# Kernel optimization log

Measured on AMD Instinct MI355X. Metric: run time of the kernel, lower is better.

The kernel has to match this reference:

```python
import jax, jax.numpy as jnp
import numpy as np

VOCAB, EMBED, HIDDEN, NCLS = 50257, 64, 64, 5
B, S = 4096, 512
BN_EPS = 1e-5


def setup_inputs() -> dict:
    key = jax.random.key(0)
    ks = jax.random.split(key, 10)
    x = jax.random.randint(ks[0], (B, S), 0, VOCAB, dtype=jnp.int64 if jax.config.jax_enable_x64 else jnp.int32)
    emb = jax.random.normal(ks[1], (VOCAB, EMBED), dtype=jnp.float32)
    emb = emb.at[0].set(0.0)  # padding_idx=0
    s = 1.0 / np.sqrt(HIDDEN)
    W_ih = jax.random.uniform(ks[2], (HIDDEN, EMBED), minval=-s, maxval=s, dtype=jnp.float32)
    W_hh = jax.random.uniform(ks[3], (HIDDEN, HIDDEN), minval=-s, maxval=s, dtype=jnp.float32)
    b_ih = jax.random.uniform(ks[4], (HIDDEN,), minval=-s, maxval=s, dtype=jnp.float32)
    b_hh = jax.random.uniform(ks[5], (HIDDEN,), minval=-s, maxval=s, dtype=jnp.float32)
    gamma = jnp.ones((HIDDEN,), dtype=jnp.float32)
    beta = jnp.zeros((HIDDEN,), dtype=jnp.float32)
    sf = 1.0 / np.sqrt(HIDDEN)
    W_fc = jax.random.uniform(ks[6], (NCLS, HIDDEN), minval=-sf, maxval=sf, dtype=jnp.float32)
    b_fc = jax.random.uniform(ks[7], (NCLS,), minval=-sf, maxval=sf, dtype=jnp.float32)
    return {"x": x, "emb": emb, "W_ih": W_ih, "W_hh": W_hh, "b_ih": b_ih,
            "b_hh": b_hh, "gamma": gamma, "beta": beta, "W_fc": W_fc, "b_fc": b_fc}


def reference(x, emb, W_ih, W_hh, b_ih, b_hh, gamma, beta, W_fc, b_fc):
    # embedding gather: [B, S, E]
    xe = emb[x]
    # precompute input projection once: [B, S, H] -> scan over time as [S, B, H]
    xp = jnp.einsum('bse,he->bsh', xe, W_ih) + b_ih + b_hh
    xp_t = jnp.swapaxes(xp, 0, 1)

    def step(h, xt):
        h = jnp.tanh(xt + h @ W_hh.T)
        return h, None

    h0 = jnp.zeros((x.shape[0], HIDDEN), dtype=xp.dtype)
    h_n, _ = jax.lax.scan(step, h0, xp_t)

    # BatchNorm1d (training-mode math: batch stats, biased variance)
    mean = jnp.mean(h_n, axis=0)
    var = jnp.mean((h_n - mean) ** 2, axis=0)
    h_bn = (h_n - mean) * jax.lax.rsqrt(var + BN_EPS) * gamma + beta
    # dropout is identity in eval / deterministic reference
    logits = h_bn @ W_fc.T + b_fc  # [B, 5]
    return logits
```

## Files before the change

kernel.cpp:

```cpp
#include <hip/hip_runtime.h>

typedef _Float16 f16;
typedef __attribute__((ext_vector_type(4))) _Float16 f16x4;
typedef __attribute__((ext_vector_type(8))) _Float16 f16x8;
typedef __attribute__((ext_vector_type(4))) float f32x4;

constexpr int BATCH  = 4096;
constexpr int SEQ    = 512;
constexpr int HID    = 64;
constexpr int EMB_N4 = 50257 * 64 / 4;
constexpr float LOG2E2 = 2.8853900817779268f;

#define MFMA_K32(a, b, c) __builtin_amdgcn_mfma_f32_16x16x32_f16(a, b, c, 0, 0, 0)

__global__ __launch_bounds__(256) void prep_kernel(
    const float4* __restrict__ emb4, const float* __restrict__ Wih,
    const float* __restrict__ Whh, f16x4* __restrict__ emb_f4,
    f16* __restrict__ wih_f, f16* __restrict__ whh_f, float* __restrict__ bn_acc)
{
  int gid = blockIdx.x * 256 + threadIdx.x;
  if (gid < EMB_N4) {
    float4 v = emb4[gid];
    f16x4 o = {(f16)v.x, (f16)v.y, (f16)v.z, (f16)v.w};
    emb_f4[gid] = o;
  } else if (gid < EMB_N4 + 1024) {
    int i0 = (gid - EMB_N4) * 4;
    #pragma unroll
    for (int k = 0; k < 4; ++k) {
      int i = i0 + k;
      wih_f[i] = (f16)(Wih[i] * LOG2E2);
      whh_f[i] = (f16)(Whh[i] * LOG2E2);
    }
  } else if (gid < EMB_N4 + 1024 + 128) {
    bn_acc[gid - (EMB_N4 + 1024)] = 0.f;
  }
}

__global__ __launch_bounds__(64, 1) void rnn_scan_kernel(
    const int* __restrict__ xx, const f16* __restrict__ emb,
    const f16* __restrict__ wih, const f16* __restrict__ whh,
    const float* __restrict__ b_ih, const float* __restrict__ b_hh,
    float* __restrict__ hT , float* __restrict__ bn_acc)
{
  const int L = threadIdx.x;
  const int n = L & 15;
  const int q = L >> 4;
  const int R0 = blockIdx.x << 4;

  f16x8 Wi[4][2], Wp[4][2];
  f32x4 bias[4];
  #pragma unroll
  for (int f = 0; f < 4; ++f) {
    const f16* wr = whh + (16 * f + n) * 64;
    #pragma unroll
    for (int h = 0; h < 2; ++h) {
      f16x4 lo = *(const f16x4*)(wr + 32 * h + 4 * q);
      f16x4 hi = *(const f16x4*)(wr + 32 * h + 16 + 4 * q);
      Wp[f][h] = __builtin_shufflevector(lo, hi, 0, 1, 2, 3, 4, 5, 6, 7);
    }
    const f16* wi = wih + (16 * f + n) * 64;
    Wi[f][0] = *(const f16x8*)(wi + 8 * q);
    Wi[f][1] = *(const f16x8*)(wi + 32 + 8 * q);
    float4 bi = *(const float4*)(b_ih + 16 * f + 4 * q);
    float4 bh = *(const float4*)(b_hh + 16 * f + 4 * q);
    f32x4 b = {(bi.x + bh.x) * LOG2E2, (bi.y + bh.y) * LOG2E2,
               (bi.z + bh.z) * LOG2E2, (bi.w + bh.w) * LOG2E2};
    bias[f] = b;
  }

  f16x8 hB01 = {0, 0, 0, 0, 0, 0, 0, 0};
  f16x8 hB23 = {0, 0, 0, 0, 0, 0, 0, 0};

  const int4* x4 = (const int4*)(xx + (R0 + n) * SEQ);
  int4 K1 = x4[1];

  f16x8 e0[4], e1[4];
  {
    int4 K0 = x4[0];
    const int id0[4] = {K0.x, K0.y, K0.z, K0.w};
    #pragma unroll
    for (int u = 0; u < 4; ++u) {
      const f16* eb = emb + (long)id0[u] * 64 + 8 * q;
      e0[u] = *(const f16x8*)(eb);
      e1[u] = *(const f16x8*)(eb + 32);
    }
  }

  for (int t = 0; t < SEQ / 4; ++t) {
    int4 K2 = x4[(t + 2 < SEQ / 4) ? t + 2 : SEQ / 4 - 1];
    const int nid[4] = {K1.x, K1.y, K1.z, K1.w};
    const bool lastt = (t == SEQ / 4 - 1);

    #pragma unroll
    for (int u = 0; u < 4; ++u) {
      f32x4 D0 = MFMA_K32(Wi[0][0], e0[u], bias[0]);
      f32x4 D1 = MFMA_K32(Wi[1][0], e0[u], bias[1]);
      f32x4 D2 = MFMA_K32(Wi[2][0], e0[u], bias[2]);
      f32x4 D3 = MFMA_K32(Wi[3][0], e0[u], bias[3]);
      D0 = MFMA_K32(Wi[0][1], e1[u], D0);
      D1 = MFMA_K32(Wi[1][1], e1[u], D1);
      D2 = MFMA_K32(Wi[2][1], e1[u], D2);
      D3 = MFMA_K32(Wi[3][1], e1[u], D3);

      {
        const f16* eb = emb + (long)nid[u] * 64 + 8 * q;
        e0[u] = *(const f16x8*)(eb);
        e1[u] = *(const f16x8*)(eb + 32);
      }

      D0 = MFMA_K32(Wp[0][0], hB01, D0);
      D1 = MFMA_K32(Wp[1][0], hB01, D1);
      D2 = MFMA_K32(Wp[2][0], hB01, D2);
      D3 = MFMA_K32(Wp[3][0], hB01, D3);
      D0 = MFMA_K32(Wp[0][1], hB23, D0);
      D1 = MFMA_K32(Wp[1][1], hB23, D1);
      D2 = MFMA_K32(Wp[2][1], hB23, D2);
      D3 = MFMA_K32(Wp[3][1], hB23, D3);

      float th[4][4];
      #pragma unroll
      for (int r = 0; r < 4; ++r) {
        float e0f = __builtin_amdgcn_exp2f(D0[r]);
        float e1f = __builtin_amdgcn_exp2f(D1[r]);
        float e2f = __builtin_amdgcn_exp2f(D2[r]);
        float e3f = __builtin_amdgcn_exp2f(D3[r]);
        th[0][r] = fmaf(-2.0f, __builtin_amdgcn_rcpf(e0f + 1.0f), 1.0f);
        th[1][r] = fmaf(-2.0f, __builtin_amdgcn_rcpf(e1f + 1.0f), 1.0f);
        th[2][r] = fmaf(-2.0f, __builtin_amdgcn_rcpf(e2f + 1.0f), 1.0f);
        th[3][r] = fmaf(-2.0f, __builtin_amdgcn_rcpf(e3f + 1.0f), 1.0f);
        hB01[r]     = (f16)th[0][r];
        hB01[4 + r] = (f16)th[1][r];
        hB23[r]     = (f16)th[2][r];
        hB23[4 + r] = (f16)th[3][r];
      }

      if (lastt && u == 3) {
        #pragma unroll
        for (int f = 0; f < 4; ++f) {
          #pragma unroll
          for (int r = 0; r < 4; ++r) {
            float v = th[f][r];
            const int feat = 16 * f + 4 * q + r;
            hT[feat * BATCH + R0 + n] = v;
            float s1 = v, s2 = v * v;
            s1 += __shfl_xor(s1, 1, 64);  s2 += __shfl_xor(s2, 1, 64);
            s1 += __shfl_xor(s1, 2, 64);  s2 += __shfl_xor(s2, 2, 64);
            s1 += __shfl_xor(s1, 4, 64);  s2 += __shfl_xor(s2, 4, 64);
            s1 += __shfl_xor(s1, 8, 64);  s2 += __shfl_xor(s2, 8, 64);
            if (n == 0) {
              atomicAdd(bn_acc + feat, s1);
              atomicAdd(bn_acc + 64 + feat, s2);
            }
          }
        }
      }
    }
    K1 = K2;
  }
}

__global__ __launch_bounds__(256) void head_kernel(
    const float* __restrict__ hT, const float* __restrict__ bn_acc,
    const float* __restrict__ gamma, const float* __restrict__ beta,
    const float* __restrict__ Wfc, const float* __restrict__ bfc,
    float* __restrict__ out)
{
  __shared__ float sc[64], sh[64];
  const int tid = threadIdx.x;
  if (tid < 64) {
    float mean = bn_acc[tid] * (1.0f / BATCH);
    float var  = bn_acc[64 + tid] * (1.0f / BATCH) - mean * mean;
    float inv  = rsqrtf(var + 1e-5f);
    float s    = gamma[tid] * inv;
    sc[tid] = s;
    sh[tid] = beta[tid] - mean * s;
  }
  __syncthreads();
  const int b = blockIdx.x * 256 + tid;
  float acc[5];
  #pragma unroll
  for (int c = 0; c < 5; ++c) acc[c] = bfc[c];
  for (int j = 0; j < HID; ++j) {
    float hv  = hT[j * BATCH + b];
    float hat = fmaf(hv, sc[j], sh[j]);
    #pragma unroll
    for (int c = 0; c < 5; ++c) acc[c] = fmaf(hat, Wfc[c * 64 + j], acc[c]);
  }
  #pragma unroll
  for (int c = 0; c < 5; ++c) out[b * 5 + c] = acc[c];
}

extern "C" void kernel_launch(void* const* d_in, const int* in_sizes, int n_in,
                              void* d_out, int out_size, void* d_ws, size_t ws_size,
                              hipStream_t stream)
{
  const int*   x     = (const int*)d_in[0];
  const float* emb   = (const float*)d_in[1];
  const float* W_ih  = (const float*)d_in[2];
  const float* W_hh  = (const float*)d_in[3];
  const float* b_ih  = (const float*)d_in[4];
  const float* b_hh  = (const float*)d_in[5];
  const float* gamma = (const float*)d_in[6];
  const float* beta  = (const float*)d_in[7];
  const float* W_fc  = (const float*)d_in[8];
  const float* b_fc  = (const float*)d_in[9];

  char* ws = (char*)d_ws;
  float* hT     = (float*)ws;
  float* bn_acc = (float*)(ws + 1048576);
  f16*   emb_f  = (f16*)(ws + 1049088);
  f16*   wih_f  = (f16*)(ws + 7481984);
  f16*   whh_f  = (f16*)(ws + 7490176);

  const int prep_items = EMB_N4 + 1024 + 128;
  prep_kernel<<<dim3((prep_items + 255) / 256), dim3(256), 0, stream>>>(
      (const float4*)emb, W_ih, W_hh, (f16x4*)emb_f, wih_f, whh_f, bn_acc);
  rnn_scan_kernel<<<dim3(BATCH / 16), dim3(64), 0, stream>>>(
      x, emb_f, wih_f, whh_f, b_ih, b_hh, hT, bn_acc);
  head_kernel<<<dim3(BATCH / 256), dim3(256), 0, stream>>>(
      hT, bn_acc, gamma, beta, W_fc, b_fc, (float*)d_out);
}
```

Baseline: 284.7 us.

## Precompute projected embedding table and split recurrence across two waves

The prep kernel now projects the whole vocabulary through W_ih plus biases once (emb·W_ih^T), so the scan gathers pre-projected rows and skips the input-projection MFMAs each step. The scan block grows to two wavefronts, each owning half of the hidden features. They exchange their halves of h through double-buffered shared memory with a barrier every timestep. This removes half the per-wave MFMA chain and all input MFMAs, but adds a workgroup barrier plus LDS round trip on the serial critical path, and a larger prep GEMM over the vocabulary.

```diff
diff --git a/kernel.cpp b/kernel.cpp
--- a/kernel.cpp
+++ b/kernel.cpp
@@ -8,83 +8,83 @@
 constexpr int BATCH  = 4096;
 constexpr int SEQ    = 512;
 constexpr int HID    = 64;
-constexpr int EMB_N4 = 50257 * 64 / 4;
+constexpr int VOCAB  = 50257;
 constexpr float LOG2E2 = 2.8853900817779268f;
 
 #define MFMA_K32(a, b, c) __builtin_amdgcn_mfma_f32_16x16x32_f16(a, b, c, 0, 0, 0)
 
 __global__ __launch_bounds__(256) void prep_kernel(
-    const float4* __restrict__ emb4, const float* __restrict__ Wih,
-    const float* __restrict__ Whh, f16x4* __restrict__ emb_f4,
-    f16* __restrict__ wih_f, f16* __restrict__ whh_f, float* __restrict__ bn_acc)
-{
-  int gid = blockIdx.x * 256 + threadIdx.x;
-  if (gid < EMB_N4) {
-    float4 v = emb4[gid];
-    f16x4 o = {(f16)v.x, (f16)v.y, (f16)v.z, (f16)v.w};
-    emb_f4[gid] = o;
-  } else if (gid < EMB_N4 + 1024) {
-    int i0 = (gid - EMB_N4) * 4;
-    #pragma unroll
-    for (int k = 0; k < 4; ++k) {
-      int i = i0 + k;
-      wih_f[i] = (f16)(Wih[i] * LOG2E2);
-      whh_f[i] = (f16)(Whh[i] * LOG2E2);
-    }
-  } else if (gid < EMB_N4 + 1024 + 128) {
-    bn_acc[gid - (EMB_N4 + 1024)] = 0.f;
-  }
-}
-
-__global__ __launch_bounds__(64, 1) void rnn_scan_kernel(
-    const int* __restrict__ xx, const f16* __restrict__ emb,
-    const f16* __restrict__ wih, const f16* __restrict__ whh,
-    const float* __restrict__ b_ih, const float* __restrict__ b_hh,
+    const float* __restrict__ emb, const float* __restrict__ Wih,
+    const float* __restrict__ Whh, const float* __restrict__ bih,
+    const float* __restrict__ bhh,
+    f16* __restrict__ embP, f16* __restrict__ whh_f, float* __restrict__ bn_acc)
+{
+  const int gid = blockIdx.x * 256 + threadIdx.x;
+  if (gid < VOCAB * 64) {
+    const int v = gid >> 6, f = gid & 63;
+    const float4* er = (const float4*)(emb + v * 64);
+    const float4* wr = (const float4*)(Wih + f * 64);
+    float acc = bih[f] + bhh[f];
+    #pragma unroll
+    for (int k = 0; k < 16; ++k) {
+      float4 e = er[k], wv = wr[k];
+      acc = fmaf(e.x, wv.x, acc); acc = fmaf(e.y, wv.y, acc);
+      acc = fmaf(e.z, wv.z, acc); acc = fmaf(e.w, wv.w, acc);
+    }
+    embP[gid] = (f16)(acc * LOG2E2);
+  } else if (gid < VOCAB * 64 + 4096) {
+    const int i = gid - VOCAB * 64;
+    whh_f[i] = (f16)(Whh[i] * LOG2E2);
+  } else if (gid < VOCAB * 64 + 4096 + 128) {
+    bn_acc[gid - (VOCAB * 64 + 4096)] = 0.f;
+  }
+}
+
+__global__ __launch_bounds__(128, 1) void rnn_scan_kernel(
+    const int* __restrict__ xx, const f16* __restrict__ embP,
+    const f16* __restrict__ whh,
     float* __restrict__ hT , float* __restrict__ bn_acc)
 {
-  const int L = threadIdx.x;
+  __shared__ int4 xslot[2][2][64];
+  const int tid = threadIdx.x;
+  const int w = tid >> 6;
+  const int L = tid & 63;
   const int n = L & 15;
   const int q = L >> 4;
   const int R0 = blockIdx.x << 4;
 
-  f16x8 Wi[4][2], Wp[4][2];
-  f32x4 bias[4];
+  f16x8 Wp[2][2];
   #pragma unroll
-  for (int f = 0; f < 4; ++f) {
-    const f16* wr = whh + (16 * f + n) * 64;
-    #pragma unroll
-    for (int h = 0; h < 2; ++h) {
-      f16x4 lo = *(const f16x4*)(wr + 32 * h + 4 * q);
-      f16x4 hi = *(const f16x4*)(wr + 32 * h + 16 + 4 * q);
-      Wp[f][h] = __builtin_shufflevector(lo, hi, 0, 1, 2, 3, 4, 5, 6, 7);
-    }
-    const f16* wi = wih + (16 * f + n) * 64;
-    Wi[f][0] = *(const f16x8*)(wi + 8 * q);
-    Wi[f][1] = *(const f16x8*)(wi + 32 + 8 * q);
-    float4 bi = *(const float4*)(b_ih + 16 * f + 4 * q);
-    float4 bh = *(const float4*)(b_hh + 16 * f + 4 * q);
-    f32x4 b = {(bi.x + bh.x) * LOG2E2, (bi.y + bh.y) * LOG2E2,
-               (bi.z + bh.z) * LOG2E2, (bi.w + bh.w) * LOG2E2};
-    bias[f] = b;
-  }
-
-  f16x8 hB01 = {0, 0, 0, 0, 0, 0, 0, 0};
-  f16x8 hB23 = {0, 0, 0, 0, 0, 0, 0, 0};
+  for (int j = 0; j < 2; ++j) {
+    const f16* wr = whh + (16 * (2 * w + j) + n) * 64;
+    #pragma unroll
+    for (int c = 0; c < 2; ++c) {
+      f16x4 lo = *(const f16x4*)(wr + 32 * c + 4 * q);
+      f16x4 hi = *(const f16x4*)(wr + 32 * c + 16 + 4 * q);
+      Wp[j][c] = __builtin_shufflevector(lo, hi, 0, 1, 2, 3, 4, 5, 6, 7);
+    }
+  }
+
+  f16x8 hOwn = {0, 0, 0, 0, 0, 0, 0, 0};
+  xslot[0][w][L] = int4{0, 0, 0, 0};
 
   const int4* x4 = (const int4*)(xx + (R0 + n) * SEQ);
   int4 K1 = x4[1];
 
-  f16x8 e0[4], e1[4];
+  const f16* ebase = embP + 32 * w + 4 * q;
+  f16x4 ep0[4], ep1[4];
   {
     int4 K0 = x4[0];
     const int id0[4] = {K0.x, K0.y, K0.z, K0.w};
     #pragma unroll
     for (int u = 0; u < 4; ++u) {
-      const f16* eb = emb + (long)id0[u] * 64 + 8 * q;
-      e0[u] = *(const f16x8*)(eb);
-      e1[u] = *(const f16x8*)(eb + 32);
-    }
-  }
+      const f16* eb = ebase + (long)id0[u] * 64;
+      ep0[u] = *(const f16x4*)(eb);
+      ep1[u] = *(const f16x4*)(eb + 16);
+    }
+  }
+
+  asm volatile("s_waitcnt lgkmcnt(0)\n\ts_barrier" ::: "memory");
 
   for (int t = 0; t < SEQ / 4; ++t) {
     int4 K2 = x4[(t + 2 < SEQ / 4) ? t + 2 : SEQ / 4 - 1];
@@ -93,54 +93,47 @@
 
     #pragma unroll
     for (int u = 0; u < 4; ++u) {
-      f32x4 D0 = MFMA_K32(Wi[0][0], e0[u], bias[0]);
-      f32x4 D1 = MFMA_K32(Wi[1][0], e0[u], bias[1]);
-      f32x4 D2 = MFMA_K32(Wi[2][0], e0[u], bias[2]);
-      f32x4 D3 = MFMA_K32(Wi[3][0], e0[u], bias[3]);
-      D0 = MFMA_K32(Wi[0][1], e1[u], D0);
-      D1 = MFMA_K32(Wi[1][1], e1[u], D1);
-      D2 = MFMA_K32(Wi[2][1], e1[u], D2);
-      D3 = MFMA_K32(Wi[3][1], e1[u], D3);
-
-      {
-        const f16* eb = emb + (long)nid[u] * 64 + 8 * q;
-        e0[u] = *(const f16x8*)(eb);
-        e1[u] = *(const f16x8*)(eb + 32);
-      }
-
-      D0 = MFMA_K32(Wp[0][0], hB01, D0);
-      D1 = MFMA_K32(Wp[1][0], hB01, D1);
-      D2 = MFMA_K32(Wp[2][0], hB01, D2);
-      D3 = MFMA_K32(Wp[3][0], hB01, D3);
-      D0 = MFMA_K32(Wp[0][1], hB23, D0);
-      D1 = MFMA_K32(Wp[1][1], hB23, D1);
-      D2 = MFMA_K32(Wp[2][1], hB23, D2);
-      D3 = MFMA_K32(Wp[3][1], hB23, D3);
-
-      float th[4][4];
+      const int p = u & 1;
+      int4 oraw = xslot[p][w ^ 1][L];
+
+      f32x4 D0, D1;
       #pragma unroll
       for (int r = 0; r < 4; ++r) {
-        float e0f = __builtin_amdgcn_exp2f(D0[r]);
-        float e1f = __builtin_amdgcn_exp2f(D1[r]);
-        float e2f = __builtin_amdgcn_exp2f(D2[r]);
-        float e3f = __builtin_amdgcn_exp2f(D3[r]);
-        th[0][r] = fmaf(-2.0f, __builtin_amdgcn_rcpf(e0f + 1.0f), 1.0f);
-        th[1][r] = fmaf(-2.0f, __builtin_amdgcn_rcpf(e1f + 1.0f), 1.0f);
-        th[2][r] = fmaf(-2.0f, __builtin_amdgcn_rcpf(e2f + 1.0f), 1.0f);
-        th[3][r] = fmaf(-2.0f, __builtin_amdgcn_rcpf(e3f + 1.0f), 1.0f);
-        hB01[r]     = (f16)th[0][r];
-        hB01[4 + r] = (f16)th[1][r];
-        hB23[r]     = (f16)th[2][r];
-        hB23[4 + r] = (f16)th[3][r];
+        D0[r] = (float)ep0[u][r];
+        D1[r] = (float)ep1[u][r];
+      }
+
+      D0 = MFMA_K32(Wp[0][w], hOwn, D0);
+      D1 = MFMA_K32(Wp[1][w], hOwn, D1);
+
+      {
+        const f16* eb = ebase + (long)nid[u] * 64;
+        ep0[u] = *(const f16x4*)(eb);
+        ep1[u] = *(const f16x4*)(eb + 16);
+      }
+
+      union { int4 i; f16x8 h; } cv; cv.i = oraw;
+      D0 = MFMA_K32(Wp[0][w ^ 1], cv.h, D0);
+      D1 = MFMA_K32(Wp[1][w ^ 1], cv.h, D1);
+
+      float th[2][4];
+      #pragma unroll
+      for (int r = 0; r < 4; ++r) {
+        float ea = __builtin_amdgcn_exp2f(D0[r]);
+        float eb2 = __builtin_amdgcn_exp2f(D1[r]);
+        th[0][r] = fmaf(-2.0f, __builtin_amdgcn_rcpf(ea + 1.0f), 1.0f);
+        th[1][r] = fmaf(-2.0f, __builtin_amdgcn_rcpf(eb2 + 1.0f), 1.0f);
+        hOwn[r]     = (f16)th[0][r];
+        hOwn[4 + r] = (f16)th[1][r];
       }
 
       if (lastt && u == 3) {
         #pragma unroll
-        for (int f = 0; f < 4; ++f) {
+        for (int j = 0; j < 2; ++j) {
           #pragma unroll
           for (int r = 0; r < 4; ++r) {
-            float v = th[f][r];
-            const int feat = 16 * f + 4 * q + r;
+            float v = th[j][r];
+            const int feat = 16 * (2 * w + j) + 4 * q + r;
             hT[feat * BATCH + R0 + n] = v;
             float s1 = v, s2 = v * v;
             s1 += __shfl_xor(s1, 1, 64);  s2 += __shfl_xor(s2, 1, 64);
@@ -154,6 +147,11 @@
           }
         }
       }
+
+      union { f16x8 h; int4 i; } cw; cw.h = hOwn;
+      xslot[p ^ 1][w][L] = cw.i;
+
+      asm volatile("s_waitcnt lgkmcnt(0)\n\ts_barrier" ::: "memory");
     }
     K1 = K2;
   }
@@ -208,15 +206,14 @@
   char* ws = (char*)d_ws;
   float* hT     = (float*)ws;
   float* bn_acc = (float*)(ws + 1048576);
-  f16*   emb_f  = (f16*)(ws + 1049088);
-  f16*   wih_f  = (f16*)(ws + 7481984);
-  f16*   whh_f  = (f16*)(ws + 7490176);
-
-  const int prep_items = EMB_N4 + 1024 + 128;
+  f16*   embP   = (f16*)(ws + 1049088);
+  f16*   whh_f  = (f16*)(ws + 7481984);
+
+  const int prep_items = VOCAB * 64 + 4096 + 128;
   prep_kernel<<<dim3((prep_items + 255) / 256), dim3(256), 0, stream>>>(
-      (const float4*)emb, W_ih, W_hh, (f16x4*)emb_f, wih_f, whh_f, bn_acc);
-  rnn_scan_kernel<<<dim3(BATCH / 16), dim3(64), 0, stream>>>(
-      x, emb_f, wih_f, whh_f, b_ih, b_hh, hT, bn_acc);
+      emb, W_ih, W_hh, b_ih, b_hh, embP, whh_f, bn_acc);
+  rnn_scan_kernel<<<dim3(BATCH / 16), dim3(128), 0, stream>>>(
+      x, embP, whh_f, hT, bn_acc);
   head_kernel<<<dim3(BATCH / 256), dim3(256), 0, stream>>>(
       hT, bn_acc, gamma, beta, W_fc, b_fc, (float*)d_out);
 }
```

Result: slower. 356.1 us (+25.1%).

## Software-pipeline input projection ahead of recurrence and batch tanh reciprocals

Applied to the files above, without the earlier changes.

Computes the input-projection MFMAs for the next timestep after the current recurrent MFMAs, so each step's dependent chain holds only the eight W_hh MFMAs and the tanh. The tanh now shares one reciprocal across four values through a prefix-product trick, with exp2 inputs clamped to avoid overflow, which cuts transcendental instructions but lengthens the dependent multiply chain. The h fragment layout is changed to interleave the f-tiles, and the W_hh register shuffle is permuted to match.

```diff
diff --git a/kernel.cpp b/kernel.cpp
--- a/kernel.cpp
+++ b/kernel.cpp
@@ -21,8 +21,7 @@
   int gid = blockIdx.x * 256 + threadIdx.x;
   if (gid < EMB_N4) {
     float4 v = emb4[gid];
-    f16x4 o = {(f16)v.x, (f16)v.y, (f16)v.z, (f16)v.w};
-    emb_f4[gid] = o;
+    emb_f4[gid] = (f16x4){(f16)v.x, (f16)v.y, (f16)v.z, (f16)v.w};
   } else if (gid < EMB_N4 + 1024) {
     int i0 = (gid - EMB_N4) * 4;
     #pragma unroll
@@ -51,21 +50,20 @@
   f32x4 bias[4];
   #pragma unroll
   for (int f = 0; f < 4; ++f) {
-    const f16* wr = whh + (16 * f + n) * 64;
-    #pragma unroll
-    for (int h = 0; h < 2; ++h) {
-      f16x4 lo = *(const f16x4*)(wr + 32 * h + 4 * q);
-      f16x4 hi = *(const f16x4*)(wr + 32 * h + 16 + 4 * q);
-      Wp[f][h] = __builtin_shufflevector(lo, hi, 0, 1, 2, 3, 4, 5, 6, 7);
-    }
     const f16* wi = wih + (16 * f + n) * 64;
     Wi[f][0] = *(const f16x8*)(wi + 8 * q);
     Wi[f][1] = *(const f16x8*)(wi + 32 + 8 * q);
+    const f16* wr = whh + (16 * f + n) * 64;
+    #pragma unroll
+    for (int c = 0; c < 2; ++c) {
+      f16x4 lo = *(const f16x4*)(wr + 32 * c + 4 * q);
+      f16x4 hi = *(const f16x4*)(wr + 32 * c + 16 + 4 * q);
+      Wp[f][c] = __builtin_shufflevector(lo, hi, 0, 4, 1, 5, 2, 6, 3, 7);
+    }
     float4 bi = *(const float4*)(b_ih + 16 * f + 4 * q);
     float4 bh = *(const float4*)(b_hh + 16 * f + 4 * q);
-    f32x4 b = {(bi.x + bh.x) * LOG2E2, (bi.y + bh.y) * LOG2E2,
-               (bi.z + bh.z) * LOG2E2, (bi.w + bh.w) * LOG2E2};
-    bias[f] = b;
+    bias[f] = (f32x4){(bi.x + bh.x) * LOG2E2, (bi.y + bh.y) * LOG2E2,
+                      (bi.z + bh.z) * LOG2E2, (bi.w + bh.w) * LOG2E2};
   }
 
   f16x8 hB01 = {0, 0, 0, 0, 0, 0, 0, 0};
@@ -86,6 +84,13 @@
     }
   }
 
+  f32x4 Dip[4];
+  #pragma unroll
+  for (int f = 0; f < 4; ++f) {
+    Dip[f] = MFMA_K32(Wi[f][0], e0[0], bias[f]);
+    Dip[f] = MFMA_K32(Wi[f][1], e1[0], Dip[f]);
+  }
+
   for (int t = 0; t < SEQ / 4; ++t) {
     int4 K2 = x4[(t + 2 < SEQ / 4) ? t + 2 : SEQ / 4 - 1];
     const int nid[4] = {K1.x, K1.y, K1.z, K1.w};
@@ -93,14 +98,23 @@
 
     #pragma unroll
     for (int u = 0; u < 4; ++u) {
-      f32x4 D0 = MFMA_K32(Wi[0][0], e0[u], bias[0]);
-      f32x4 D1 = MFMA_K32(Wi[1][0], e0[u], bias[1]);
-      f32x4 D2 = MFMA_K32(Wi[2][0], e0[u], bias[2]);
-      f32x4 D3 = MFMA_K32(Wi[3][0], e0[u], bias[3]);
-      D0 = MFMA_K32(Wi[0][1], e1[u], D0);
-      D1 = MFMA_K32(Wi[1][1], e1[u], D1);
-      D2 = MFMA_K32(Wi[2][1], e1[u], D2);
-      D3 = MFMA_K32(Wi[3][1], e1[u], D3);
+      f32x4 D0 = MFMA_K32(Wp[0][0], hB01, Dip[0]);
+      f32x4 D1 = MFMA_K32(Wp[1][0], hB01, Dip[1]);
+      f32x4 D2 = MFMA_K32(Wp[2][0], hB01, Dip[2]);
+      f32x4 D3 = MFMA_K32(Wp[3][0], hB01, Dip[3]);
+      D0 = MFMA_K32(Wp[0][1], hB23, D0);
+      D1 = MFMA_K32(Wp[1][1], hB23, D1);
+      D2 = MFMA_K32(Wp[2][1], hB23, D2);
+      D3 = MFMA_K32(Wp[3][1], hB23, D3);
+
+      {
+        const int v = (u + 1) & 3;
+        #pragma unroll
+        for (int f = 0; f < 4; ++f) {
+          Dip[f] = MFMA_K32(Wi[f][0], e0[v], bias[f]);
+          Dip[f] = MFMA_K32(Wi[f][1], e1[v], Dip[f]);
+        }
+      }
 
       {
         const f16* eb = emb + (long)nid[u] * 64 + 8 * q;
@@ -108,30 +122,32 @@
         e1[u] = *(const f16x8*)(eb + 32);
       }
 
-      D0 = MFMA_K32(Wp[0][0], hB01, D0);
-      D1 = MFMA_K32(Wp[1][0], hB01, D1);
-      D2 = MFMA_K32(Wp[2][0], hB01, D2);
-      D3 = MFMA_K32(Wp[3][0], hB01, D3);
-      D0 = MFMA_K32(Wp[0][1], hB23, D0);
-      D1 = MFMA_K32(Wp[1][1], hB23, D1);
-      D2 = MFMA_K32(Wp[2][1], hB23, D2);
-      D3 = MFMA_K32(Wp[3][1], hB23, D3);
-
       float th[4][4];
       #pragma unroll
+      for (int f = 0; f < 4; ++f) {
+        const f32x4 Df = (f == 0) ? D0 : (f == 1) ? D1 : (f == 2) ? D2 : D3;
+        float A0 = __builtin_amdgcn_exp2f(fminf(Df[0], 16.0f)) + 1.0f;
+        float A1 = __builtin_amdgcn_exp2f(fminf(Df[1], 16.0f)) + 1.0f;
+        float A2 = __builtin_amdgcn_exp2f(fminf(Df[2], 16.0f)) + 1.0f;
+        float A3 = __builtin_amdgcn_exp2f(fminf(Df[3], 16.0f)) + 1.0f;
+        float t1 = A0 * A1, t2 = t1 * A2, t3 = t2 * A3;
+        float rr = __builtin_amdgcn_rcpf(t3);
+        float i3 = rr * t2;
+        float s3 = rr * A3;
+        float i2 = s3 * t1;
+        float s2 = s3 * A2;
+        th[f][0] = fmaf(-2.0f, s2 * A1, 1.0f);
+        th[f][1] = fmaf(-2.0f, s2 * A0, 1.0f);
+        th[f][2] = fmaf(-2.0f, i2, 1.0f);
+        th[f][3] = fmaf(-2.0f, i3, 1.0f);
+      }
+
+      #pragma unroll
       for (int r = 0; r < 4; ++r) {
-        float e0f = __builtin_amdgcn_exp2f(D0[r]);
-        float e1f = __builtin_amdgcn_exp2f(D1[r]);
-        float e2f = __builtin_amdgcn_exp2f(D2[r]);
-        float e3f = __builtin_amdgcn_exp2f(D3[r]);
-        th[0][r] = fmaf(-2.0f, __builtin_amdgcn_rcpf(e0f + 1.0f), 1.0f);
-        th[1][r] = fmaf(-2.0f, __builtin_amdgcn_rcpf(e1f + 1.0f), 1.0f);
-        th[2][r] = fmaf(-2.0f, __builtin_amdgcn_rcpf(e2f + 1.0f), 1.0f);
-        th[3][r] = fmaf(-2.0f, __builtin_amdgcn_rcpf(e3f + 1.0f), 1.0f);
-        hB01[r]     = (f16)th[0][r];
-        hB01[4 + r] = (f16)th[1][r];
-        hB23[r]     = (f16)th[2][r];
-        hB23[4 + r] = (f16)th[3][r];
+        hB01[2 * r]     = (f16)th[0][r];
+        hB01[2 * r + 1] = (f16)th[1][r];
+        hB23[2 * r]     = (f16)th[2][r];
+        hB23[2 * r + 1] = (f16)th[3][r];
       }
 
       if (lastt && u == 3) {
```

After: 325.8 us. +14.4%, slower.
